# Optimization experiments

Measured on AMD Instinct MI355X. Metric: run time of the kernel, lower is better.

The kernel has to match this reference:

```python
import jax, jax.numpy as jnp
import numpy as np

BN_EPS = 1e-5
DIST_EPS = 1e-8


def setup_inputs() -> dict:
    key = jax.random.key(0)
    ks = jax.random.split(key, 10)
    B, Ni, Mi = 4, 16384, 4096
    C1, C2 = 64, 64
    Cin = C1 + C2  # 128, mlp=[128,128,128]
    inp = {
        "unknown": jax.random.normal(ks[0], (B * Ni, 3), dtype=jnp.float32),
        "unknown_batch_cnt": np.full(B, Ni, dtype=np.int64),
        "known": jax.random.normal(ks[1], (B * Mi, 3), dtype=jnp.float32),
        "known_batch_cnt": np.full(B, Mi, dtype=np.int64),
        "unknown_feats": jax.random.normal(ks[2], (B * Ni, C1), dtype=jnp.float32),
        "known_feats": jax.random.normal(ks[3], (B * Mi, C2), dtype=jnp.float32),
        "W1": jax.random.normal(ks[4], (128, Cin), dtype=jnp.float32) * 0.05,
        "g1": jnp.ones((128,), dtype=jnp.float32),
        "b1": jnp.zeros((128,), dtype=jnp.float32),
        "W2": jax.random.normal(ks[5], (128, 128), dtype=jnp.float32) * 0.05,
        "g2": jnp.ones((128,), dtype=jnp.float32),
        "b2": jnp.zeros((128,), dtype=jnp.float32),
    }
    return inp


def _three_nn(u, k):
    # u: (B,Ni,3), k: (B,Mi,3) -> dist (B,Ni,3), idx (B,Ni,3) within each batch
    d2 = (jnp.sum(u * u, -1)[:, :, None] + jnp.sum(k * k, -1)[:, None, :]
          - 2.0 * jnp.einsum("bnd,bmd->bnm", u, k))  # (B,Ni,Mi)
    neg_d2, idx = jax.lax.top_k(-d2, 3)
    dist = jnp.sqrt(jnp.maximum(-neg_d2, 0.0))
    return dist, idx


def _bn_relu(y, g, b):
    # BatchNorm2d over the point dim (training-mode batch stats), then ReLU
    mu = jnp.mean(y, axis=0)
    var = jnp.mean((y - mu) ** 2, axis=0)
    return jax.nn.relu((y - mu) * jax.lax.rsqrt(var + BN_EPS) * g + b)


def reference(unknown, unknown_batch_cnt, known, known_batch_cnt,
              unknown_feats, known_feats, W1, g1, b1, W2, g2, b2):
    ucnt = np.asarray(unknown_batch_cnt)
    kcnt = np.asarray(known_batch_cnt)
    B = ucnt.shape[0]
    Ni, Mi = int(ucnt[0]), int(kcnt[0])  # equal-count ragged batches
    C2 = known_feats.shape[1]

    u = unknown.reshape(B, Ni, 3)
    k = known.reshape(B, Mi, 3)
    dist, idx = _three_nn(u, k)

    dist_recip = 1.0 / (dist + DIST_EPS)
    weight = dist_recip / jnp.sum(dist_recip, axis=-1, keepdims=True)  # (B,Ni,3)

    kf = known_feats.reshape(B, Mi, C2)
    gathered = kf[jnp.arange(B)[:, None, None], idx]  # (B,Ni,3,C2)
    interp = jnp.sum(weight[..., None] * gathered, axis=2).reshape(B * Ni, C2)

    x = jnp.concatenate([interp, unknown_feats], axis=1)  # (N, C2+C1)
    x = _bn_relu(x @ W1.T, g1, b1)
    x = _bn_relu(x @ W2.T, g2, b2)
    return x
```

## Files before the change

### kernel.cpp

```cpp
#include <hip/hip_runtime.h>
#include <hip/hip_bf16.h>

#define GRID  32
#define NCELL (GRID * GRID * GRID)
#define H     0.3125f
#define INVH  3.2f
#define OFF   5.0f
#define SUBW  8
#define XPAD  136
#define NREP  16

using f32x4  = __attribute__((ext_vector_type(4))) float;
using bf16x8 = __attribute__((ext_vector_type(8))) short;

static __device__ inline short f2bs(float f) {
  __hip_bfloat16 h = __float2bfloat16(f);
  return __builtin_bit_cast(short, h);
}
static __device__ inline float bs2f(short s) {
  return __bfloat162float(__builtin_bit_cast(__hip_bfloat16, s));
}
static __device__ inline int cellco(float x) {
  int c = (int)((x + OFF) * INVH);
  return min(GRID - 1, max(0, c));
}

#define INSF(dv, mv)                                   \
  {                                                    \
    bool q0 = dv < b0, q1 = dv < b1, q2 = dv < b2;     \
    float P0 = b0, P1 = b1; int Q0 = j0, Q1 = j1;      \
    b2 = q1 ? P1 : (q2 ? dv : b2);                     \
    j2 = q1 ? Q1 : (q2 ? mv : j2);                     \
    b1 = q0 ? P0 : (q1 ? dv : P1);                     \
    j1 = q0 ? Q0 : (q1 ? mv : Q1);                     \
    b0 = q0 ? dv : P0;                                 \
    j0 = q0 ? mv : Q0;                                 \
  }

#define MERGE3(lo_mk, hi_mk)                                                        \
  for (int mk = lo_mk; mk <= hi_mk; mk <<= 1) {                                     \
    float ob0 = __shfl_xor(b0, mk), ob1 = __shfl_xor(b1, mk), ob2 = __shfl_xor(b2, mk); \
    int   oj0 = __shfl_xor(j0, mk), oj1 = __shfl_xor(j1, mk), oj2 = __shfl_xor(j2, mk); \
    INSF(ob0, oj0); INSF(ob1, oj1); INSF(ob2, oj2);                                 \
  }

__global__ __launch_bounds__(256) void zero_k(int4* __restrict__ dst, int n4) {
  int i = blockIdx.x * 256 + threadIdx.x;
  if (i < n4) dst[i] = int4{0, 0, 0, 0};
}

__global__ __launch_bounds__(256) void hist_k(
    const float* __restrict__ known, int Mtot, int Mi,
    const float* __restrict__ unknown, int Ntot,
    int* __restrict__ khist, int* __restrict__ qhist,
    int* __restrict__ kcell, int* __restrict__ qcell,
    const float* __restrict__ W1, const float* __restrict__ W2,
    __hip_bfloat16* __restrict__ Wb1, __hip_bfloat16* __restrict__ Wb2) {
  int i = blockIdx.x * 256 + threadIdx.x;
  if (i < 128 * 128) {
    Wb1[i] = __float2bfloat16(W1[i]);
    Wb2[i] = __float2bfloat16(W2[i]);
  }
  if (i < Mtot) {
    int b = i / Mi;
    float x = known[(size_t)i * 3], y = known[(size_t)i * 3 + 1], z = known[(size_t)i * 3 + 2];
    int c = b * NCELL + (cellco(z) * GRID + cellco(y)) * GRID + cellco(x);
    kcell[i] = c;
    atomicAdd(&khist[c], 1);
  }
  if (i < Ntot) {
    int Ni = Ntot / (Mtot / Mi);
    int b = i / Ni;
    float x = unknown[(size_t)i * 3], y = unknown[(size_t)i * 3 + 1], z = unknown[(size_t)i * 3 + 2];
    int c = b * NCELL + (cellco(z) * GRID + cellco(y)) * GRID + cellco(x);
    qcell[i] = c;
    atomicAdd(&qhist[c], 1);
  }
}

__global__ __launch_bounds__(256) void scan1_k(
    const int4* __restrict__ Hc4, int* __restrict__ bsum) {
  __shared__ int sh[256];
  int t = threadIdx.x;
  int4 h = Hc4[blockIdx.x * 256 + t];
  int s = h.x + h.y + h.z + h.w;
  sh[t] = s;
  __syncthreads();
  for (int d = 128; d > 0; d >>= 1) {
    if (t < d) sh[t] += sh[t + d];
    __syncthreads();
  }
  if (t == 0) bsum[blockIdx.x] = sh[0];
}

__global__ __launch_bounds__(256) void scan2_k(
    int* __restrict__ bsum, int nb, int* __restrict__ kstart, int* __restrict__ qstart,
    int nc, int Mtot, int Ntot) {
  __shared__ int sh[256];
  int t = threadIdx.x;
  int v = (t < nb) ? bsum[t] : 0;
  sh[t] = v;
  __syncthreads();
  for (int d = 1; d < 256; d <<= 1) {
    int u = (t >= d) ? sh[t - d] : 0;
    __syncthreads();
    sh[t] += u;
    __syncthreads();
  }
  if (t < nb) bsum[t] = sh[t] - v;
  if (t == 0) { kstart[nc] = Mtot; qstart[nc] = Ntot; }
}

__global__ __launch_bounds__(256) void scan3_k(
    const int4* __restrict__ Hc4, const int* __restrict__ bsum,
    int* __restrict__ kstart, int* __restrict__ kfill,
    int* __restrict__ qstart, int* __restrict__ qfill, int nc, int Mtot) {
  __shared__ int sh[256];
  int t = threadIdx.x;
  int g4 = blockIdx.x * 256 + t;
  int4 h = Hc4[g4];
  int s = h.x + h.y + h.z + h.w;
  sh[t] = s;
  __syncthreads();
  for (int d = 1; d < 256; d <<= 1) {
    int u = (t >= d) ? sh[t - d] : 0;
    __syncthreads();
    sh[t] += u;
    __syncthreads();
  }
  int run = bsum[blockIdx.x] + sh[t] - s;
  int hv[4] = {h.x, h.y, h.z, h.w};
#pragma unroll
  for (int j = 0; j < 4; ++j) {
    int g = g4 * 4 + j;
    if (g < nc) { kstart[g] = run; kfill[g] = run; }
    else        { int q = g - nc; qstart[q] = run - Mtot; qfill[q] = run - Mtot; }
    run += hv[j];
  }
}

__global__ __launch_bounds__(256) void scatter_k(
    const float* __restrict__ known, int Mtot, int Mi,
    const float* __restrict__ unknown, int Ntot,
    const int* __restrict__ kcell, const int* __restrict__ qcell,
    int* __restrict__ kfill, int* __restrict__ qfill,
    f32x4* __restrict__ k4s, int* __restrict__ korder,
    f32x4* __restrict__ u4s, int* __restrict__ qorder) {
  int i = blockIdx.x * 256 + threadIdx.x;
  if (i < Mtot) {
    int slot = atomicAdd(&kfill[kcell[i]], 1);
    float x = known[(size_t)i * 3], y = known[(size_t)i * 3 + 1], z = known[(size_t)i * 3 + 2];
    f32x4 v;
    v[0] = -2.f * x; v[1] = -2.f * y; v[2] = -2.f * z;
    v[3] = x * x + y * y + z * z;
    k4s[slot] = v;
    korder[slot] = i - (i / Mi) * Mi;
  }
  if (i < Ntot) {
    int slot = atomicAdd(&qfill[qcell[i]], 1);
    float x = unknown[(size_t)i * 3], y = unknown[(size_t)i * 3 + 1], z = unknown[(size_t)i * 3 + 2];
    f32x4 v;
    v[0] = x; v[1] = y; v[2] = z;
    v[3] = __fmaf_rn(x, x, __fmaf_rn(y, y, z * z));
    u4s[slot] = v;
    qorder[slot] = i;
  }
}

static __device__ __forceinline__ void scan_box_strided(
    int R, int sub, int stride, int cx, int cy, int cz, int cellbase,
    const int* __restrict__ cstart, const f32x4* __restrict__ k4s,
    const int* __restrict__ korder,
    float ux, float uy, float uz,
    float& b0, float& b1, float& b2, int& j0, int& j1, int& j2) {
  int zlo = max(cz - R, 0), zhi = min(cz + R, GRID - 1);
  int ylo = max(cy - R, 0), yhi = min(cy + R, GRID - 1);
  int xlo = max(cx - R, 0), xhi = min(cx + R, GRID - 1);
  int ny = yhi - ylo + 1;
  int nrows = (zhi - zlo + 1) * ny;
  for (int rid = sub; rid < nrows; rid += stride) {
    int zz = rid / ny;
    int y  = ylo + (rid - zz * ny);
    int row = cellbase + ((zlo + zz) * GRID + y) * GRID;
    int s = cstart[row + xlo];
    int e = cstart[row + xhi + 1];
    for (int i = s; i < e; ++i) {
      f32x4 k = k4s[i];
      float d = __fmaf_rn(ux, k[0], __fmaf_rn(uy, k[1], __fmaf_rn(uz, k[2], k[3])));
      int m = korder[i];
      INSF(d, m);
    }
  }
}

__global__ __launch_bounds__(256) void knn_grid_k(
    const f32x4* __restrict__ u4s, const int* __restrict__ qorder,
    const int* __restrict__ cstart, const f32x4* __restrict__ k4s,
    const int* __restrict__ korder, int Ni,
    float* __restrict__ w, int* __restrict__ idx,
    int* __restrict__ rcnt, int* __restrict__ rlist, float* __restrict__ rd3) {
  int nwc = gridDim.x * 4;
  int gw  = blockIdx.x * 4 + (threadIdx.x >> 6);
  int wchunk = (gw * 997) & (nwc - 1);
  int s   = wchunk * 8 + ((threadIdx.x & 63) / SUBW);
  int sub = threadIdx.x & (SUBW - 1);
  f32x4 u4 = u4s[s];
  int p = qorder[s];
  int b = p / Ni;
  float ux = u4[0], uy = u4[1], uz = u4[2], uu = u4[3];
  int cx = cellco(ux), cy = cellco(uy), cz = cellco(uz);
  int cellbase = b * NCELL;
  int xlo = max(cx - 1, 0), xhi = min(cx + 1, GRID - 1);

  int cs[9], ce[9];
#pragma unroll
  for (int q = 0; q < 9; ++q) {
    int z = cz + (q / 3) - 1;
    int y = cy + (q % 3) - 1;
    bool valid = ((unsigned)z < GRID) && ((unsigned)y < GRID);
    int row = cellbase + (z * GRID + y) * GRID;
    int a0 = valid ? row + xlo : cellbase;
    int a1 = valid ? row + xhi + 1 : cellbase;
    cs[q] = cstart[a0];
    ce[q] = cstart[a1];
  }

  float b0 = 3e38f, b1 = 3e38f, b2 = 3e38f;
  int   j0 = 0,     j1 = 0,     j2 = 0;
#pragma unroll
  for (int q = 0; q < 9; ++q) {
    for (int i = cs[q] + sub; i < ce[q]; i += SUBW) {
      f32x4 k = k4s[i];
      float d = __fmaf_rn(ux, k[0], __fmaf_rn(uy, k[1], __fmaf_rn(uz, k[2], k[3])));
      int m = korder[i];
      INSF(d, m);
    }
  }
  MERGE3(1, SUBW / 2);

  float d3sq = b2 + uu;
  bool ok = d3sq <= H * H;

  if (sub == 0) {
    if (ok) {
      float d0 = sqrtf(fmaxf(b0 + uu, 0.f));
      float d1 = sqrtf(fmaxf(b1 + uu, 0.f));
      float d2 = sqrtf(fmaxf(b2 + uu, 0.f));
      float r0 = 1.f / (d0 + 1e-8f);
      float r1 = 1.f / (d1 + 1e-8f);
      float r2 = 1.f / (d2 + 1e-8f);
      float rs = 1.f / (r0 + r1 + r2);
      size_t o = (size_t)p * 3;
      w[o] = r0 * rs; w[o + 1] = r1 * rs; w[o + 2] = r2 * rs;
      idx[o] = j0; idx[o + 1] = j1; idx[o + 2] = j2;
    } else {
      int t = atomicAdd(rcnt, 1);
      rlist[t] = s;
      rd3[t] = d3sq;
    }
  }
}

__global__ __launch_bounds__(256) void knn_retry_k(
    const f32x4* __restrict__ u4s, const int* __restrict__ qorder,
    const int* __restrict__ rlist, const float* __restrict__ rd3,
    const int* __restrict__ rcnt,
    const int* __restrict__ cstart, const f32x4* __restrict__ k4s,
    const int* __restrict__ korder, int Ni,
    float* __restrict__ w, int* __restrict__ idx) {
  int lane = threadIdx.x & 63;
  int wv   = blockIdx.x * 4 + (threadIdx.x >> 6);
  int nw   = gridDim.x * 4;
  int cnt  = rcnt[0];
  for (int q = wv; q < cnt; q += nw) {
    int sq = rlist[q];
    f32x4 u4 = u4s[sq];
    int p = qorder[sq];
    int b = p / Ni;
    float ux = u4[0], uy = u4[1], uz = u4[2], uu = u4[3];
    int cx = cellco(ux), cy = cellco(uy), cz = cellco(uz);
    int cellbase = b * NCELL;

    float d3sq = rd3[q];
    int Rc = 1;
    float b0, b1, b2; int j0, j1, j2;
    bool ok = false;
    while (!ok) {
      if (d3sq < 1e30f) {
        Rc = max((int)ceilf(sqrtf(fmaxf(d3sq, 0.f)) * INVH), Rc + 1);
      } else {
        Rc = Rc * 2;
      }
      Rc = min(Rc, GRID);
      b0 = b1 = b2 = 3e38f; j0 = j1 = j2 = 0;
      scan_box_strided(Rc, lane, 64, cx, cy, cz, cellbase, cstart, k4s, korder,
                       ux, uy, uz, b0, b1, b2, j0, j1, j2);
      MERGE3(1, 32);
      d3sq = b2 + uu;
      float cov = (float)Rc * H;
      ok = (d3sq <= cov * cov) || (Rc >= GRID);
    }
    if (lane == 0) {
      float d0 = sqrtf(fmaxf(b0 + uu, 0.f));
      float d1 = sqrtf(fmaxf(b1 + uu, 0.f));
      float d2 = sqrtf(fmaxf(b2 + uu, 0.f));
      float r0 = 1.f / (d0 + 1e-8f);
      float r1 = 1.f / (d1 + 1e-8f);
      float r2 = 1.f / (d2 + 1e-8f);
      float rs = 1.f / (r0 + r1 + r2);
      size_t o = (size_t)p * 3;
      w[o] = r0 * rs; w[o + 1] = r1 * rs; w[o + 2] = r2 * rs;
      idx[o] = j0; idx[o + 1] = j1; idx[o + 2] = j2;
    }
  }
}

template <bool F32OUT>
static __device__ __forceinline__ void gemm_half(
    const short* xs, const short* Ws, int row0,
    float* yf, __hip_bfloat16* yb, float* ls, float* lq) {
  int t = threadIdx.x;
  int lane = t & 63;
  int wv = t >> 6;
  int r = lane & 15, g = lane >> 4;
  int tile = wv >> 1, half = wv & 1;
  int trow = tile * 16;

  bf16x8 a[4];
#pragma unroll
  for (int q = 0; q < 4; ++q)
    a[q] = *reinterpret_cast<const bf16x8*>(&xs[(trow + r) * XPAD + g * 8 + q * 32]);

  int orow = row0 + trow + g * 4;
#pragma unroll
  for (int ct = 0; ct < 4; ++ct) {
    int ocol = half * 64 + ct * 16 + r;
    f32x4 acc = {0.f, 0.f, 0.f, 0.f};
    size_t bbase = (size_t)ocol * 128 + g * 8;
#pragma unroll
    for (int q = 0; q < 4; ++q) {
      bf16x8 bfr = *reinterpret_cast<const bf16x8*>(Ws + bbase + q * 32);
      acc = __builtin_amdgcn_mfma_f32_16x16x32_bf16(a[q], bfr, acc, 0, 0, 0);
    }
    if (F32OUT) {
#pragma unroll
      for (int i = 0; i < 4; ++i)
        yf[(size_t)(orow + i) * 128 + ocol] = acc[i];
    } else {
#pragma unroll
      for (int i = 0; i < 4; ++i)
        yb[(size_t)(orow + i) * 128 + ocol] = __float2bfloat16(acc[i]);
    }
    float s  = acc[0] + acc[1] + acc[2] + acc[3];
    float q2 = acc[0] * acc[0] + acc[1] * acc[1] + acc[2] * acc[2] + acc[3] * acc[3];
    s  += __shfl_xor(s, 16);  s  += __shfl_xor(s, 32);
    q2 += __shfl_xor(q2, 16); q2 += __shfl_xor(q2, 32);
    if (g == 0) {
      atomicAdd(&ls[ocol], s);
      atomicAdd(&lq[ocol], q2);
    }
  }
}

__global__ __launch_bounds__(256) void gemm1_fused_k(
    const float* __restrict__ kf, const float* __restrict__ uf,
    const float* __restrict__ wgt, const int* __restrict__ idx,
    const __hip_bfloat16* __restrict__ Wb, __hip_bfloat16* __restrict__ Yb,
    float* __restrict__ stats, int Ni, int Mi) {
  __shared__ short xs[32 * XPAD];
  __shared__ float ls[128], lq[128];
  int t = threadIdx.x;
  if (t < 128) { ls[t] = 0.f; lq[t] = 0.f; }
  int row0 = blockIdx.x * 32;

  int rr = t >> 3, c0 = (t & 7) * 16;
  int p = row0 + rr;
  short tmp[16];
  if (c0 < 64) {
    size_t o = (size_t)p * 3;
    float w0 = wgt[o], w1 = wgt[o + 1], w2 = wgt[o + 2];
    int i0 = idx[o], i1 = idx[o + 1], i2 = idx[o + 2];
    int b = p / Ni;
    const float* kfb = kf + (size_t)b * Mi * 64 + c0;
    const f32x4* r0p = reinterpret_cast<const f32x4*>(kfb + (size_t)i0 * 64);
    const f32x4* r1p = reinterpret_cast<const f32x4*>(kfb + (size_t)i1 * 64);
    const f32x4* r2p = reinterpret_cast<const f32x4*>(kfb + (size_t)i2 * 64);
#pragma unroll
    for (int j = 0; j < 4; ++j) {
      f32x4 av = r0p[j], bv = r1p[j], cv = r2p[j];
#pragma unroll
      for (int e = 0; e < 4; ++e)
        tmp[j * 4 + e] = f2bs(w0 * av[e] + w1 * bv[e] + w2 * cv[e]);
    }
  } else {
    const f32x4* ufp = reinterpret_cast<const f32x4*>(uf + (size_t)p * 64 + (c0 - 64));
#pragma unroll
    for (int j = 0; j < 4; ++j) {
      f32x4 av = ufp[j];
#pragma unroll
      for (int e = 0; e < 4; ++e)
        tmp[j * 4 + e] = f2bs(av[e]);
    }
  }
  *reinterpret_cast<bf16x8*>(&xs[rr * XPAD + c0])     = *reinterpret_cast<bf16x8*>(&tmp[0]);
  *reinterpret_cast<bf16x8*>(&xs[rr * XPAD + c0 + 8]) = *reinterpret_cast<bf16x8*>(&tmp[8]);
  __syncthreads();

  gemm_half<false>(xs, reinterpret_cast<const short*>(Wb), row0, nullptr, Yb, ls, lq);

  __syncthreads();
  if (t < 128) {
    int rep = blockIdx.x & (NREP - 1);
    atomicAdd(&stats[rep * 256 + t], ls[t]);
    atomicAdd(&stats[rep * 256 + 128 + t], lq[t]);
  }
}

__global__ __launch_bounds__(256) void gemm2_bn_k(
    const __hip_bfloat16* __restrict__ Y1, const float* __restrict__ AB,
    const __hip_bfloat16* __restrict__ Wb, float* __restrict__ Yf,
    float* __restrict__ stats) {
  __shared__ short xs[32 * XPAD];
  __shared__ float ls[128], lq[128];
  int t = threadIdx.x;
  if (t < 128) { ls[t] = 0.f; lq[t] = 0.f; }
  int row0 = blockIdx.x * 32;

  int rr = t >> 3, c0 = (t & 7) * 16;
  int p = row0 + rr;
  const short* Ys = reinterpret_cast<const short*>(Y1);
  bf16x8 v0 = *reinterpret_cast<const bf16x8*>(Ys + (size_t)p * 128 + c0);
  bf16x8 v1 = *reinterpret_cast<const bf16x8*>(Ys + (size_t)p * 128 + c0 + 8);
  short tmp[16];
#pragma unroll
  for (int j = 0; j < 8; ++j)
    tmp[j] = f2bs(fmaxf(bs2f(v0[j]) * AB[c0 + j] + AB[128 + c0 + j], 0.f));
#pragma unroll
  for (int j = 0; j < 8; ++j)
    tmp[8 + j] = f2bs(fmaxf(bs2f(v1[j]) * AB[c0 + 8 + j] + AB[128 + c0 + 8 + j], 0.f));
  *reinterpret_cast<bf16x8*>(&xs[rr * XPAD + c0])     = *reinterpret_cast<bf16x8*>(&tmp[0]);
  *reinterpret_cast<bf16x8*>(&xs[rr * XPAD + c0 + 8]) = *reinterpret_cast<bf16x8*>(&tmp[8]);
  __syncthreads();

  gemm_half<true>(xs, reinterpret_cast<const short*>(Wb), row0, Yf, nullptr, ls, lq);

  __syncthreads();
  if (t < 128) {
    int rep = blockIdx.x & (NREP - 1);
    atomicAdd(&stats[rep * 256 + t], ls[t]);
    atomicAdd(&stats[rep * 256 + 128 + t], lq[t]);
  }
}

__global__ void finalize_k(const float* __restrict__ stats, const float* __restrict__ g,
                           const float* __restrict__ bb, float invN, float* __restrict__ AB) {
  int c = threadIdx.x;
  float s = 0.f, q = 0.f;
  for (int rpl = 0; rpl < NREP; ++rpl) {
    s += stats[rpl * 256 + c];
    q += stats[rpl * 256 + 128 + c];
  }
  float mu  = s * invN;
  float var = q * invN - mu * mu;
  float A = rsqrtf(var + 1e-5f) * g[c];
  AB[c] = A;
  AB[128 + c] = bb[c] - mu * A;
}

__global__ __launch_bounds__(256) void bnrelu_f32_k(
    float* __restrict__ Y, const float* __restrict__ AB, long n4) {
  long i = (long)blockIdx.x * 256 + threadIdx.x;
  long stride = (long)gridDim.x * 256;
  for (; i < n4; i += stride) {
    f32x4 y = reinterpret_cast<f32x4*>(Y)[i];
    int c0 = (int)((i * 4) & 127);
    f32x4 A  = *reinterpret_cast<const f32x4*>(AB + c0);
    f32x4 Bv = *reinterpret_cast<const f32x4*>(AB + 128 + c0);
    f32x4 o;
#pragma unroll
    for (int j = 0; j < 4; ++j) o[j] = fmaxf(y[j] * A[j] + Bv[j], 0.f);
    reinterpret_cast<f32x4*>(Y)[i] = o;
  }
}

extern "C" void kernel_launch(void* const* d_in, const int* in_sizes, int n_in,
                              void* d_out, int out_size, void* d_ws, size_t ws_size,
                              hipStream_t stream) {
  const float* unknown = (const float*)d_in[0];
  const float* known   = (const float*)d_in[2];
  const float* uf      = (const float*)d_in[4];
  const float* kf      = (const float*)d_in[5];
  const float* W1      = (const float*)d_in[6];
  const float* g1      = (const float*)d_in[7];
  const float* b1      = (const float*)d_in[8];
  const float* W2      = (const float*)d_in[9];
  const float* g2      = (const float*)d_in[10];
  const float* b2      = (const float*)d_in[11];

  int B    = in_sizes[1];
  int Ntot = in_sizes[0] / 3;
  int Mtot = in_sizes[2] / 3;
  int Ni = Ntot / B, Mi = Mtot / B;
  int nc = B * NCELL;
  int n2 = 2 * nc;

  char* ws = (char*)d_ws;
  size_t off = 0;
  auto alloc = [&](size_t bytes) {
    void* p = ws + off;
    off += (bytes + 255) & ~(size_t)255;
    return p;
  };
  float* stats  = (float*)alloc(2 * NREP * 256 * 4);
  int*   rcnt   = (int*)alloc(4);
  int*   khist  = (int*)alloc((size_t)n2 * 4);
  int*   qhist  = khist + nc;
  size_t zero_bytes = (size_t)((char*)(khist + n2) - (char*)stats);
  int*   kstart = (int*)alloc((size_t)(nc + 1) * 4);
  int*   qstart = (int*)alloc((size_t)(nc + 1) * 4);
  int*   kfill  = (int*)alloc((size_t)nc * 4);
  int*   qfill  = (int*)alloc((size_t)nc * 4);
  int*   kcell  = (int*)alloc((size_t)Mtot * 4);
  int*   qcell  = (int*)alloc((size_t)Ntot * 4);
  int*   korder = (int*)alloc((size_t)Mtot * 4);
  int*   qorder = (int*)alloc((size_t)Ntot * 4);
  int*   bsum   = (int*)alloc((size_t)(n2 / 1024) * 4);
  int*   rlist  = (int*)alloc((size_t)Ntot * 4);
  float* rd3    = (float*)alloc((size_t)Ntot * 4);
  f32x4* k4s    = (f32x4*)alloc((size_t)Mtot * 16);
  f32x4* u4s    = (f32x4*)alloc((size_t)Ntot * 16);
  float* wgt    = (float*)alloc((size_t)Ntot * 3 * 4);
  int*   idx    = (int*)alloc((size_t)Ntot * 3 * 4);
  __hip_bfloat16* y1b = (__hip_bfloat16*)alloc((size_t)Ntot * 128 * 2);
  __hip_bfloat16* Wb1 = (__hip_bfloat16*)alloc(128 * 128 * 2);
  __hip_bfloat16* Wb2 = (__hip_bfloat16*)alloc(128 * 128 * 2);
  float* AB1 = (float*)alloc(256 * 4);
  float* AB2 = (float*)alloc(256 * 4);

  float* y2 = (float*)d_out;
  long n4 = (long)Ntot * 128 / 4;
  float invN = 1.0f / (float)Ntot;
  int nb = n2 / 1024;
  float* stats2 = stats + NREP * 256;
  int zn4 = (int)(zero_bytes / 16);

  zero_k<<<(zn4 + 255) / 256, 256, 0, stream>>>((int4*)stats, zn4);
  hist_k<<<(Ntot + 255) / 256, 256, 0, stream>>>(known, Mtot, Mi, unknown, Ntot,
                                                 khist, qhist, kcell, qcell, W1, W2, Wb1, Wb2);
  scan1_k<<<nb, 256, 0, stream>>>((const int4*)khist, bsum);
  scan2_k<<<1, 256, 0, stream>>>(bsum, nb, kstart, qstart, nc, Mtot, Ntot);
  scan3_k<<<nb, 256, 0, stream>>>((const int4*)khist, bsum, kstart, kfill, qstart, qfill, nc, Mtot);
  scatter_k<<<(Ntot + 255) / 256, 256, 0, stream>>>(known, Mtot, Mi, unknown, Ntot,
                                                    kcell, qcell, kfill, qfill, k4s, korder, u4s, qorder);
  knn_grid_k<<<Ntot / 32, 256, 0, stream>>>(u4s, qorder, kstart, k4s, korder, Ni,
                                            wgt, idx, rcnt, rlist, rd3);
  knn_retry_k<<<1024, 256, 0, stream>>>(u4s, qorder, rlist, rd3, rcnt,
                                        kstart, k4s, korder, Ni, wgt, idx);
  gemm1_fused_k<<<Ntot / 32, 256, 0, stream>>>(kf, uf, wgt, idx, Wb1, y1b, stats, Ni, Mi);
  finalize_k<<<1, 128, 0, stream>>>(stats, g1, b1, invN, AB1);
  gemm2_bn_k<<<Ntot / 32, 256, 0, stream>>>(y1b, AB1, Wb2, y2, stats2);
  finalize_k<<<1, 128, 0, stream>>>(stats2, g2, b2, invN, AB2);
  bnrelu_f32_k<<<2048, 256, 0, stream>>>(y2, AB2, n4);
}
```

Measured before the change: 159.9 us.

## Merge scan kernels, tighten kNN acceptance radius, dual-accumulate kNN, bf16 intermediate

Folds the single-block scan2 into scan3, so each block redundantly scans the block sums and one launch is removed. The kNN grid search gets a per-query coverage radius based on the query's position within its cell, which widens the acceptance test so fewer queries fall through to the retry path. Its inner loop also processes two candidates per iteration into two independent top-3 lists to expose more ILP. The second GEMM now writes a bf16 intermediate that the final BN+ReLU kernel expands to fp32, halving that intermediate's traffic at some cost in precision.

```diff
diff --git a/kernel.cpp b/kernel.cpp
--- a/kernel.cpp
+++ b/kernel.cpp
@@ -25,17 +25,18 @@
   return min(GRID - 1, max(0, c));
 }
 
-#define INSF(dv, mv)                                   \
+#define INS3(B0, B1, B2, J0, J1, J2, dv, mv)           \
   {                                                    \
-    bool q0 = dv < b0, q1 = dv < b1, q2 = dv < b2;     \
-    float P0 = b0, P1 = b1; int Q0 = j0, Q1 = j1;      \
-    b2 = q1 ? P1 : (q2 ? dv : b2);                     \
-    j2 = q1 ? Q1 : (q2 ? mv : j2);                     \
-    b1 = q0 ? P0 : (q1 ? dv : P1);                     \
-    j1 = q0 ? Q0 : (q1 ? mv : Q1);                     \
-    b0 = q0 ? dv : P0;                                 \
-    j0 = q0 ? mv : Q0;                                 \
-  }
+    bool q0 = dv < B0, q1 = dv < B1, q2 = dv < B2;     \
+    float P0 = B0, P1 = B1; int Q0 = J0, Q1 = J1;      \
+    B2 = q1 ? P1 : (q2 ? dv : B2);                     \
+    J2 = q1 ? Q1 : (q2 ? mv : J2);                     \
+    B1 = q0 ? P0 : (q1 ? dv : P1);                     \
+    J1 = q0 ? Q0 : (q1 ? mv : Q1);                     \
+    B0 = q0 ? dv : P0;                                 \
+    J0 = q0 ? mv : Q0;                                 \
+  }
+#define INSF(dv, mv) INS3(b0, b1, b2, j0, j1, j2, dv, mv)
 
 #define MERGE3(lo_mk, hi_mk)                                                        \
   for (int mk = lo_mk; mk <= hi_mk; mk <<= 1) {                                     \
@@ -93,42 +94,31 @@
   if (t == 0) bsum[blockIdx.x] = sh[0];
 }
 
-__global__ __launch_bounds__(256) void scan2_k(
-    int* __restrict__ bsum, int nb, int* __restrict__ kstart, int* __restrict__ qstart,
+__global__ __launch_bounds__(256) void scan3_k(
+    const int4* __restrict__ Hc4, const int* __restrict__ bsum, int nbk,
+    int* __restrict__ kstart, int* __restrict__ kfill,
+    int* __restrict__ qstart, int* __restrict__ qfill,
     int nc, int Mtot, int Ntot) {
   __shared__ int sh[256];
+  __shared__ int sv[256], sc[256];
   int t = threadIdx.x;
-  int v = (t < nb) ? bsum[t] : 0;
-  sh[t] = v;
-  __syncthreads();
-  for (int d = 1; d < 256; d <<= 1) {
-    int u = (t >= d) ? sh[t - d] : 0;
-    __syncthreads();
-    sh[t] += u;
-    __syncthreads();
-  }
-  if (t < nb) bsum[t] = sh[t] - v;
-  if (t == 0) { kstart[nc] = Mtot; qstart[nc] = Ntot; }
-}
-
-__global__ __launch_bounds__(256) void scan3_k(
-    const int4* __restrict__ Hc4, const int* __restrict__ bsum,
-    int* __restrict__ kstart, int* __restrict__ kfill,
-    int* __restrict__ qstart, int* __restrict__ qfill, int nc, int Mtot) {
-  __shared__ int sh[256];
-  int t = threadIdx.x;
+  int v = (t < nbk) ? bsum[t] : 0;
+  sv[t] = v; sc[t] = v;
   int g4 = blockIdx.x * 256 + t;
   int4 h = Hc4[g4];
   int s = h.x + h.y + h.z + h.w;
   sh[t] = s;
   __syncthreads();
   for (int d = 1; d < 256; d <<= 1) {
-    int u = (t >= d) ? sh[t - d] : 0;
+    int u1 = (t >= d) ? sc[t - d] : 0;
+    int u2 = (t >= d) ? sh[t - d] : 0;
     __syncthreads();
-    sh[t] += u;
+    sc[t] += u1;
+    sh[t] += u2;
     __syncthreads();
   }
-  int run = bsum[blockIdx.x] + sh[t] - s;
+  int blockbase = sc[blockIdx.x] - sv[blockIdx.x];
+  int run = blockbase + sh[t] - s;
   int hv[4] = {h.x, h.y, h.z, h.w};
 #pragma unroll
   for (int j = 0; j < 4; ++j) {
@@ -137,6 +127,7 @@
     else        { int q = g - nc; qstart[q] = run - Mtot; qfill[q] = run - Mtot; }
     run += hv[j];
   }
+  if (blockIdx.x == 0 && t == 0) { kstart[nc] = Mtot; qstart[nc] = Ntot; }
 }
 
 __global__ __launch_bounds__(256) void scatter_k(
@@ -212,6 +203,14 @@
   int cellbase = b * NCELL;
   int xlo = max(cx - 1, 0), xhi = min(cx + 1, GRID - 1);
 
+  float fx = (ux + OFF) * INVH - cx;
+  float fy = (uy + OFF) * INVH - cy;
+  float fz = (uz + OFF) * INVH - cz;
+  float mf = fminf(fminf(fminf(fx, 1.f - fx), fminf(fy, 1.f - fy)),
+                   fminf(fz, 1.f - fz));
+  float cov = H * (1.f + fmaxf(mf, 0.f));
+  float covsq = cov * cov;
+
   int cs[9], ce[9];
 #pragma unroll
   for (int q = 0; q < 9; ++q) {
@@ -227,19 +226,34 @@
 
   float b0 = 3e38f, b1 = 3e38f, b2 = 3e38f;
   int   j0 = 0,     j1 = 0,     j2 = 0;
+  float e0 = 3e38f, e1 = 3e38f, e2 = 3e38f;
+  int   f0 = 0,     f1 = 0,     f2 = 0;
 #pragma unroll
   for (int q = 0; q < 9; ++q) {
-    for (int i = cs[q] + sub; i < ce[q]; i += SUBW) {
-      f32x4 k = k4s[i];
-      float d = __fmaf_rn(ux, k[0], __fmaf_rn(uy, k[1], __fmaf_rn(uz, k[2], k[3])));
-      int m = korder[i];
-      INSF(d, m);
-    }
-  }
+    int i = cs[q] + sub;
+    int e = ce[q];
+    for (; i + SUBW < e; i += 2 * SUBW) {
+      f32x4 kA = k4s[i];
+      f32x4 kB = k4s[i + SUBW];
+      int mA = korder[i];
+      int mB = korder[i + SUBW];
+      float dA = __fmaf_rn(ux, kA[0], __fmaf_rn(uy, kA[1], __fmaf_rn(uz, kA[2], kA[3])));
+      float dB = __fmaf_rn(ux, kB[0], __fmaf_rn(uy, kB[1], __fmaf_rn(uz, kB[2], kB[3])));
+      INS3(b0, b1, b2, j0, j1, j2, dA, mA);
+      INS3(e0, e1, e2, f0, f1, f2, dB, mB);
+    }
+    if (i < e) {
+      f32x4 kA = k4s[i];
+      int mA = korder[i];
+      float dA = __fmaf_rn(ux, kA[0], __fmaf_rn(uy, kA[1], __fmaf_rn(uz, kA[2], kA[3])));
+      INS3(b0, b1, b2, j0, j1, j2, dA, mA);
+    }
+  }
+  INSF(e0, f0); INSF(e1, f1); INSF(e2, f2);
   MERGE3(1, SUBW / 2);
 
   float d3sq = b2 + uu;
-  bool ok = d3sq <= H * H;
+  bool ok = d3sq <= covsq;
 
   if (sub == 0) {
     if (ok) {
@@ -418,7 +432,7 @@
 
 __global__ __launch_bounds__(256) void gemm2_bn_k(
     const __hip_bfloat16* __restrict__ Y1, const float* __restrict__ AB,
-    const __hip_bfloat16* __restrict__ Wb, float* __restrict__ Yf,
+    const __hip_bfloat16* __restrict__ Wb, __hip_bfloat16* __restrict__ Yb2,
     float* __restrict__ stats) {
   __shared__ short xs[32 * XPAD];
   __shared__ float ls[128], lq[128];
@@ -442,7 +456,7 @@
   *reinterpret_cast<bf16x8*>(&xs[rr * XPAD + c0 + 8]) = *reinterpret_cast<bf16x8*>(&tmp[8]);
   __syncthreads();
 
-  gemm_half<true>(xs, reinterpret_cast<const short*>(Wb), row0, Yf, nullptr, ls, lq);
+  gemm_half<false>(xs, reinterpret_cast<const short*>(Wb), row0, nullptr, Yb2, ls, lq);
 
   __syncthreads();
   if (t < 128) {
@@ -467,19 +481,24 @@
   AB[128 + c] = bb[c] - mu * A;
 }
 
-__global__ __launch_bounds__(256) void bnrelu_f32_k(
-    float* __restrict__ Y, const float* __restrict__ AB, long n4) {
+__global__ __launch_bounds__(256) void bnrelu_out_k(
+    const __hip_bfloat16* __restrict__ Y, const float* __restrict__ AB,
+    float* __restrict__ Out, long n8) {
   long i = (long)blockIdx.x * 256 + threadIdx.x;
   long stride = (long)gridDim.x * 256;
-  for (; i < n4; i += stride) {
-    f32x4 y = reinterpret_cast<f32x4*>(Y)[i];
-    int c0 = (int)((i * 4) & 127);
-    f32x4 A  = *reinterpret_cast<const f32x4*>(AB + c0);
-    f32x4 Bv = *reinterpret_cast<const f32x4*>(AB + 128 + c0);
-    f32x4 o;
-#pragma unroll
-    for (int j = 0; j < 4; ++j) o[j] = fmaxf(y[j] * A[j] + Bv[j], 0.f);
-    reinterpret_cast<f32x4*>(Y)[i] = o;
+  const bf16x8* Y8 = reinterpret_cast<const bf16x8*>(Y);
+  for (; i < n8; i += stride) {
+    bf16x8 y = Y8[i];
+    int c0 = (int)((i * 8) & 127);
+    f32x4 o0, o1;
+#pragma unroll
+    for (int j = 0; j < 4; ++j)
+      o0[j] = fmaxf(bs2f(y[j]) * AB[c0 + j] + AB[128 + c0 + j], 0.f);
+#pragma unroll
+    for (int j = 0; j < 4; ++j)
+      o1[j] = fmaxf(bs2f(y[4 + j]) * AB[c0 + 4 + j] + AB[128 + c0 + 4 + j], 0.f);
+    reinterpret_cast<f32x4*>(Out)[i * 2]     = o0;
+    reinterpret_cast<f32x4*>(Out)[i * 2 + 1] = o1;
   }
 }
 
@@ -532,13 +551,14 @@
   float* wgt    = (float*)alloc((size_t)Ntot * 3 * 4);
   int*   idx    = (int*)alloc((size_t)Ntot * 3 * 4);
   __hip_bfloat16* y1b = (__hip_bfloat16*)alloc((size_t)Ntot * 128 * 2);
+  __hip_bfloat16* y2b = (__hip_bfloat16*)alloc((size_t)Ntot * 128 * 2);
   __hip_bfloat16* Wb1 = (__hip_bfloat16*)alloc(128 * 128 * 2);
   __hip_bfloat16* Wb2 = (__hip_bfloat16*)alloc(128 * 128 * 2);
   float* AB1 = (float*)alloc(256 * 4);
   float* AB2 = (float*)alloc(256 * 4);
 
   float* y2 = (float*)d_out;
-  long n4 = (long)Ntot * 128 / 4;
+  long n8 = (long)Ntot * 128 / 8;
   float invN = 1.0f / (float)Ntot;
   int nb = n2 / 1024;
   float* stats2 = stats + NREP * 256;
@@ -548,8 +568,8 @@
   hist_k<<<(Ntot + 255) / 256, 256, 0, stream>>>(known, Mtot, Mi, unknown, Ntot,
                                                  khist, qhist, kcell, qcell, W1, W2, Wb1, Wb2);
   scan1_k<<<nb, 256, 0, stream>>>((const int4*)khist, bsum);
-  scan2_k<<<1, 256, 0, stream>>>(bsum, nb, kstart, qstart, nc, Mtot, Ntot);
-  scan3_k<<<nb, 256, 0, stream>>>((const int4*)khist, bsum, kstart, kfill, qstart, qfill, nc, Mtot);
+  scan3_k<<<nb, 256, 0, stream>>>((const int4*)khist, bsum, nb, kstart, kfill,
+                                  qstart, qfill, nc, Mtot, Ntot);
   scatter_k<<<(Ntot + 255) / 256, 256, 0, stream>>>(known, Mtot, Mi, unknown, Ntot,
                                                     kcell, qcell, kfill, qfill, k4s, korder, u4s, qorder);
   knn_grid_k<<<Ntot / 32, 256, 0, stream>>>(u4s, qorder, kstart, k4s, korder, Ni,
@@ -558,7 +578,7 @@
                                         kstart, k4s, korder, Ni, wgt, idx);
   gemm1_fused_k<<<Ntot / 32, 256, 0, stream>>>(kf, uf, wgt, idx, Wb1, y1b, stats, Ni, Mi);
   finalize_k<<<1, 128, 0, stream>>>(stats, g1, b1, invN, AB1);
-  gemm2_bn_k<<<Ntot / 32, 256, 0, stream>>>(y1b, AB1, Wb2, y2, stats2);
+  gemm2_bn_k<<<Ntot / 32, 256, 0, stream>>>(y1b, AB1, Wb2, y2b, stats2);
   finalize_k<<<1, 128, 0, stream>>>(stats2, g2, b2, invN, AB2);
-  bnrelu_f32_k<<<2048, 256, 0, stream>>>(y2, AB2, n4);
-}
+  bnrelu_out_k<<<2048, 256, 0, stream>>>(y2b, AB2, y2, n8);
+}
```

After: 149.2 us. 6.7% less time.
